# Performance work log

Hardware: AMD Instinct MI355X
Metric: run time of the kernel (lower is better)

Reference implementation:

```python
import jax, jax.numpy as jnp
import numpy as np


def setup_inputs() -> dict:
    key = jax.random.key(0)
    k1, k2 = jax.random.split(key)
    B, H, N, C = 8, 8, 2048, 64
    x = jax.random.normal(k1, (B, H, N, C), dtype=jnp.float32)
    # torch nn.Linear(dim, 3*dim) weight layout: [3C, C]
    W_qkv = jax.random.normal(k2, (3 * C, C), dtype=jnp.float32) * (C ** -0.5)
    return {"x": x, "W_qkv": W_qkv}


def reference(x, W_qkv):
    B, H, N, C = x.shape
    scale = C ** -0.5
    # fused qkv projection: x @ W^T, then split
    qkv = jnp.einsum('bhnc,dc->bhnd', x, W_qkv)  # [B,H,N,3C]
    q, k, v = jnp.split(qkv, 3, axis=-1)
    # full N x N score matrix (matches the naive original)
    attn = jnp.einsum('bhnc,bhmc->bhnm', q, k) * scale
    attn = jax.nn.softmax(attn, axis=-1)
    out = jnp.einsum('bhnm,bhmc->bhnc', attn, v)  # [B,H,N,C]
    # head-mixing shuffle: reshape(B,H,N,H,C//H).transpose(1,3).reshape(B,H,N,C)
    out = out.reshape(B, H, N, H, C // H)
    out = out.transpose(0, 3, 2, 1, 4)
    return out.reshape(B, H, N, C)
```

## Files before the change

### kernel.cpp

```cpp
#include <hip/hip_runtime.h>
#include <math.h>

#define BH    64
#define NSEQ  2048
#define CDIM  64
#define WSTR  72

typedef unsigned short ushort_t;
typedef __attribute__((ext_vector_type(8))) short short8;
typedef __attribute__((ext_vector_type(4))) float float4v;

__device__ __forceinline__ ushort_t f32_to_bf16_rne(float x) {
  unsigned int u = __float_as_uint(x);
  u += 0x7fffu + ((u >> 16) & 1u);
  return (ushort_t)(u >> 16);
}

__device__ __forceinline__ unsigned int cvtpk(float a, float b) {
  unsigned int r;
  asm("v_cvt_pk_bf16_f32 %0, %1, %2" : "=v"(r) : "v"(a), "v"(b));
  return r;
}

__device__ __forceinline__ void glds16(const ushort_t* g, ushort_t* l) {
  __builtin_amdgcn_global_load_lds(
      (const __attribute__((address_space(1))) void*)g,
      (__attribute__((address_space(3))) void*)l, 16, 0, 0);
}

__global__ __launch_bounds__(256) void qkv_proj_mfma(
    const float* __restrict__ x, const float* __restrict__ w,
    ushort_t* __restrict__ q, ushort_t* __restrict__ k,
    ushort_t* __restrict__ vt) {
  __shared__ ushort_t Wb[192 * WSTR];
  ushort_t* Sg = Wb;
  const int t = threadIdx.x;
  const int lane = t & 63, wv = t >> 6;
  const int quad = lane >> 4, l16 = lane & 15;
  const long rowbase = (long)blockIdx.x * 128;
  const int head  = (int)(rowbase >> 11);
  const int nbase = (int)(rowbase & 2047);

  for (int u = t; u < 1536; u += 256) {
    const int d = u >> 3, o8 = (u & 7) * 8;
    const float sc = (d < 64) ? 0.1803368801111244f : 1.0f;
    const float4 f0 = *reinterpret_cast<const float4*>(w + d * 64 + o8);
    const float4 f1 = *reinterpret_cast<const float4*>(w + d * 64 + o8 + 4);
    ushort_t tmp[8] __attribute__((aligned(16)));
    tmp[0] = f32_to_bf16_rne(f0.x * sc); tmp[1] = f32_to_bf16_rne(f0.y * sc);
    tmp[2] = f32_to_bf16_rne(f0.z * sc); tmp[3] = f32_to_bf16_rne(f0.w * sc);
    tmp[4] = f32_to_bf16_rne(f1.x * sc); tmp[5] = f32_to_bf16_rne(f1.y * sc);
    tmp[6] = f32_to_bf16_rne(f1.z * sc); tmp[7] = f32_to_bf16_rne(f1.w * sc);
    *reinterpret_cast<uint4*>(&Wb[d * WSTR + o8]) = *reinterpret_cast<const uint4*>(tmp);
  }
  __syncthreads();

  short8 xf[2][2];
#pragma unroll
  for (int tm = 0; tm < 2; ++tm)
#pragma unroll
    for (int kb = 0; kb < 2; ++kb) {
      const float* xp = x + (rowbase + wv * 32 + tm * 16 + l16) * 64 + kb * 32 + quad * 8;
      const float4 f0 = *reinterpret_cast<const float4*>(xp);
      const float4 f1 = *reinterpret_cast<const float4*>(xp + 4);
      ushort_t tmp[8] __attribute__((aligned(16)));
      tmp[0] = f32_to_bf16_rne(f0.x); tmp[1] = f32_to_bf16_rne(f0.y);
      tmp[2] = f32_to_bf16_rne(f0.z); tmp[3] = f32_to_bf16_rne(f0.w);
      tmp[4] = f32_to_bf16_rne(f1.x); tmp[5] = f32_to_bf16_rne(f1.y);
      tmp[6] = f32_to_bf16_rne(f1.z); tmp[7] = f32_to_bf16_rne(f1.w);
      xf[tm][kb] = *reinterpret_cast<const short8*>(tmp);
    }

  float4v aqk[8][2];
  float4v av[2][4];
#pragma unroll
  for (int nt = 0; nt < 8; ++nt)
#pragma unroll
    for (int tm = 0; tm < 2; ++tm)
#pragma unroll
      for (int r = 0; r < 4; ++r) aqk[nt][tm][r] = 0.f;
#pragma unroll
  for (int tm = 0; tm < 2; ++tm)
#pragma unroll
    for (int nt = 0; nt < 4; ++nt)
#pragma unroll
      for (int r = 0; r < 4; ++r) av[tm][nt][r] = 0.f;

#pragma unroll
  for (int kb = 0; kb < 2; ++kb) {
#pragma unroll
    for (int nt = 0; nt < 8; ++nt) {
      const short8 wf = *reinterpret_cast<const short8*>(
          &Wb[(nt * 16 + l16) * WSTR + kb * 32 + quad * 8]);
      aqk[nt][0] = __builtin_amdgcn_mfma_f32_16x16x32_bf16(wf, xf[0][kb], aqk[nt][0], 0, 0, 0);
      aqk[nt][1] = __builtin_amdgcn_mfma_f32_16x16x32_bf16(wf, xf[1][kb], aqk[nt][1], 0, 0, 0);
    }
#pragma unroll
    for (int nt = 0; nt < 4; ++nt) {
      const short8 wfv = *reinterpret_cast<const short8*>(
          &Wb[((128 + nt * 16) + l16) * WSTR + kb * 32 + quad * 8]);
      av[0][nt] = __builtin_amdgcn_mfma_f32_16x16x32_bf16(xf[0][kb], wfv, av[0][nt], 0, 0, 0);
      av[1][nt] = __builtin_amdgcn_mfma_f32_16x16x32_bf16(xf[1][kb], wfv, av[1][nt], 0, 0, 0);
    }
  }

  __syncthreads();

#pragma unroll
  for (int tm = 0; tm < 2; ++tm) {
    const int row = wv * 32 + tm * 16 + l16;
#pragma unroll
    for (int nt = 0; nt < 4; ++nt) {
      const int dchunk = nt * 2 + (quad >> 1);
      uint2 pk;
      pk.x = cvtpk(aqk[nt][tm][0], aqk[nt][tm][1]);
      pk.y = cvtpk(aqk[nt][tm][2], aqk[nt][tm][3]);
      *reinterpret_cast<uint2*>(
          &Sg[row * 64 + ((dchunk ^ (row & 7)) * 8) + (quad & 1) * 4]) = pk;
    }
  }
  __syncthreads();
#pragma unroll
  for (int i = 0; i < 4; ++i) {
    const int g = i * 256 + t;
    const int row = g >> 3, ch = g & 7;
    const uint4 v = *reinterpret_cast<const uint4*>(
        &Sg[row * 64 + ((ch ^ (row & 7)) * 8)]);
    *reinterpret_cast<uint4*>(q + (rowbase + row) * 64 + ch * 8) = v;
  }
  __syncthreads();

#pragma unroll
  for (int tm = 0; tm < 2; ++tm) {
    const int row = wv * 32 + tm * 16 + l16;
#pragma unroll
    for (int nt = 4; nt < 8; ++nt) {
      const int dchunk = (nt - 4) * 2 + (quad >> 1);
      uint2 pk;
      pk.x = cvtpk(aqk[nt][tm][0], aqk[nt][tm][1]);
      pk.y = cvtpk(aqk[nt][tm][2], aqk[nt][tm][3]);
      *reinterpret_cast<uint2*>(
          &Sg[row * 64 + ((dchunk ^ (row & 7)) * 8) + (quad & 1) * 4]) = pk;
    }
  }
  __syncthreads();
#pragma unroll
  for (int i = 0; i < 4; ++i) {
    const int g = i * 256 + t;
    const int row = g >> 3, ch = g & 7;
    const uint4 v = *reinterpret_cast<const uint4*>(
        &Sg[row * 64 + ((ch ^ (row & 7)) * 8)]);
    *reinterpret_cast<uint4*>(k + (rowbase + row) * 64 + ch * 8) = v;
  }
  __syncthreads();

#pragma unroll
  for (int tm = 0; tm < 2; ++tm)
#pragma unroll
    for (int nt = 0; nt < 4; ++nt) {
      const int c = nt * 16 + l16;
      const int nchunk = wv * 4 + tm * 2 + (quad >> 1);
      uint2 pk;
      pk.x = cvtpk(av[tm][nt][0], av[tm][nt][1]);
      pk.y = cvtpk(av[tm][nt][2], av[tm][nt][3]);
      *reinterpret_cast<uint2*>(
          &Sg[c * 128 + ((nchunk ^ (c & 15)) * 8) + (quad & 1) * 4]) = pk;
    }
  __syncthreads();
#pragma unroll
  for (int i = 0; i < 4; ++i) {
    const int g = i * 256 + t;
    const int c = g >> 4, ch = g & 15;
    const uint4 v = *reinterpret_cast<const uint4*>(
        &Sg[c * 128 + ((ch ^ (c & 15)) * 8)]);
    *reinterpret_cast<uint4*>(vt + (long)head * (64 * 2048) + (long)c * 2048 +
                              nbase + ch * 8) = v;
  }
}

__global__ __launch_bounds__(512, 4) void flash_attn_mfma(
    const ushort_t* __restrict__ q, const ushort_t* __restrict__ k,
    const ushort_t* __restrict__ vt, float* __restrict__ out) {
  __shared__ ushort_t Ks2[2][32 * 64];
  __shared__ ushort_t Vs2[2][64 * 32];
  __shared__ ushort_t Ps[256 * 32];
  const int t = threadIdx.x;
  const int lane = t & 63, w = t >> 6;
  const int quad = lane >> 4, l16 = lane & 15;
  const int id = blockIdx.x;
  const int qt = id >> 6;
  const int bh = ((id & 7) << 3) | ((id >> 3) & 7);
  const long hoff = (long)bh * NSEQ * CDIM;
  const ushort_t* qp  = q  + hoff + (long)qt * 256 * CDIM;
  const ushort_t* kp  = k  + hoff;
  const ushort_t* vtp = vt + hoff;

  short8 qf[2][2];
#pragma unroll
  for (int tm = 0; tm < 2; ++tm)
#pragma unroll
    for (int kb = 0; kb < 2; ++kb)
      qf[tm][kb] = *reinterpret_cast<const short8*>(
          qp + (w * 32 + tm * 16 + l16) * 64 + kb * 32 + quad * 8);

  float4v O[4][2];
  float rs[2];
  rs[0] = 0.f; rs[1] = 0.f;
#pragma unroll
  for (int ct = 0; ct < 4; ++ct)
#pragma unroll
    for (int tm = 0; tm < 2; ++tm)
#pragma unroll
      for (int r = 0; r < 4; ++r) O[ct][tm][r] = 0.f;

  const int ws = w & 3;
  const bool isK = (w < 4);
  const int krow = ws * 8 + (lane >> 3);
  const int kchk = (lane & 7) ^ (lane >> 3);
  const int kdst = ws * 8 * 64;
  const int vrow = ws * 16 + (lane >> 2);
  const int vchk = (lane & 3) ^ ((lane >> 3) & 3);
  const int vdst = ws * 16 * 32;
  const int pswz = (l16 >> 1) & 3;

  if (isK) glds16(kp + (long)krow * 64 + kchk * 8, &Ks2[0][kdst]);
  else     glds16(vtp + (long)vrow * 2048 + vchk * 8, &Vs2[0][vdst]);

  for (int tile = 0; tile < NSEQ / 32; ++tile) {
    const int cur = tile & 1;
    __syncthreads();
    if (tile < NSEQ / 32 - 1) {
      const long nxt = tile + 1;
      if (isK) glds16(kp + (nxt * 32 + krow) * 64 + kchk * 8, &Ks2[1 - cur][kdst]);
      else     glds16(vtp + (long)vrow * 2048 + nxt * 32 + vchk * 8, &Vs2[1 - cur][vdst]);
    }

    float4v s[2][2];
#pragma unroll
    for (int nt = 0; nt < 2; ++nt)
#pragma unroll
      for (int tm = 0; tm < 2; ++tm)
#pragma unroll
        for (int r = 0; r < 4; ++r) s[nt][tm][r] = 0.f;

#pragma unroll
    for (int kb = 0; kb < 2; ++kb) {
      short8 kf[2];
#pragma unroll
      for (int nt = 0; nt < 2; ++nt)
        kf[nt] = *reinterpret_cast<const short8*>(
            &Ks2[cur][(nt * 16 + l16) * 64 + (((kb * 4 + quad) ^ (l16 & 7)) * 8)]);
#pragma unroll
      for (int nt = 0; nt < 2; ++nt)
#pragma unroll
        for (int tm = 0; tm < 2; ++tm)
          s[nt][tm] = __builtin_amdgcn_mfma_f32_16x16x32_bf16(
              kf[nt], qf[tm][kb], s[nt][tm], 0, 0, 0);
    }

#pragma unroll
    for (int tm = 0; tm < 2; ++tm)
#pragma unroll
      for (int nt = 0; nt < 2; ++nt) {
        const float p0 = __builtin_amdgcn_exp2f(s[nt][tm][0]);
        const float p1 = __builtin_amdgcn_exp2f(s[nt][tm][1]);
        const float p2 = __builtin_amdgcn_exp2f(s[nt][tm][2]);
        const float p3 = __builtin_amdgcn_exp2f(s[nt][tm][3]);
        rs[tm] += (p0 + p1) + (p2 + p3);
        uint2 pk;
        pk.x = cvtpk(p0, p1);
        pk.y = cvtpk(p2, p3);
        *reinterpret_cast<uint2*>(
            &Ps[(w * 32 + tm * 16 + l16) * 32 +
                (((nt * 2 + (quad >> 1)) ^ pswz) * 8) + (quad & 1) * 4]) = pk;
      }

    {
      short8 pf[2], vf[4];
#pragma unroll
      for (int tm = 0; tm < 2; ++tm)
        pf[tm] = *reinterpret_cast<const short8*>(
            &Ps[(w * 32 + tm * 16 + l16) * 32 + ((quad ^ pswz) * 8)]);
#pragma unroll
      for (int ct = 0; ct < 4; ++ct)
        vf[ct] = *reinterpret_cast<const short8*>(
            &Vs2[cur][(ct * 16 + l16) * 32 + ((quad ^ pswz) * 8)]);
#pragma unroll
      for (int ct = 0; ct < 4; ++ct)
#pragma unroll
        for (int tm = 0; tm < 2; ++tm)
          O[ct][tm] = __builtin_amdgcn_mfma_f32_16x16x32_bf16(
              vf[ct], pf[tm], O[ct][tm], 0, 0, 0);
    }
  }

  const int bi = bh >> 3, h = bh & 7;
  float inv[2];
#pragma unroll
  for (int tm = 0; tm < 2; ++tm) {
    float l = rs[tm];
    l += __shfl_xor(l, 16, 64);
    l += __shfl_xor(l, 32, 64);
    inv[tm] = 1.f / l;
  }
#pragma unroll
  for (int ct = 0; ct < 4; ++ct)
#pragma unroll
    for (int tm = 0; tm < 2; ++tm) {
      const int n = qt * 256 + w * 32 + tm * 16 + l16;
      const int h2 = ct * 2 + (quad >> 1);
      const int c2b = (quad & 1) * 4;
      float4 v4;
      v4.x = O[ct][tm][0] * inv[tm]; v4.y = O[ct][tm][1] * inv[tm];
      v4.z = O[ct][tm][2] * inv[tm]; v4.w = O[ct][tm][3] * inv[tm];
      *reinterpret_cast<float4*>(
          &out[(((long)(bi * 8 + h2)) * NSEQ + n) * 64 + h * 8 + c2b]) = v4;
    }
}

extern "C" void kernel_launch(void* const* d_in, const int* in_sizes, int n_in,
                              void* d_out, int out_size, void* d_ws, size_t ws_size,
                              hipStream_t stream) {
  (void)in_sizes; (void)n_in; (void)out_size; (void)ws_size;
  const float* x = (const float*)d_in[0];
  const float* w = (const float*)d_in[1];
  float* out = (float*)d_out;

  ushort_t* qws  = (ushort_t*)d_ws;
  ushort_t* kws  = qws + (size_t)BH * NSEQ * CDIM;
  ushort_t* vtws = kws + (size_t)BH * NSEQ * CDIM;

  qkv_proj_mfma<<<(BH * NSEQ) / 128, 256, 0, stream>>>(x, w, qws, kws, vtws);
  flash_attn_mfma<<<512, 512, 0, stream>>>(qws, kws, vtws, out);
}
```

Baseline: 164.5 us.

## Precompute swizzled bf16 weight image once and async-load it; raise MFMA priority

Adds a tiny one-block kernel that converts, scales and XOR-swizzles W_qkv into a bf16 image once, stored in the tail of the output buffer, which the flash kernel later overwrites. Each of the 1024 projection blocks then copies that image straight into LDS with global_load_lds, overlapped with the x conversion, instead of converting fp32 weights per block. It also wraps the MFMA groups in the attention loop with s_setprio to favour matrix issue. The cost is an extra kernel launch and reliance on output-buffer scratch being overwritten later.

Result: no change. 166.1 us (+1.0%).

```diff
diff --git a/kernel.cpp b/kernel.cpp
--- a/kernel.cpp
+++ b/kernel.cpp
@@ -4,7 +4,6 @@
 #define BH    64
 #define NSEQ  2048
 #define CDIM  64
-#define WSTR  72
 
 typedef unsigned short ushort_t;
 typedef __attribute__((ext_vector_type(8))) short short8;
@@ -28,11 +27,30 @@
       (__attribute__((address_space(3))) void*)l, 16, 0, 0);
 }
 
+__global__ __launch_bounds__(256) void w_prep(
+    const float* __restrict__ w, ushort_t* __restrict__ wimg) {
+  const int t = threadIdx.x;
+#pragma unroll
+  for (int i = 0; i < 6; ++i) {
+    const int idx = i * 256 + t;
+    const int d = idx >> 3, ch = idx & 7;
+    const float sc = (d < 64) ? 0.1803368801111244f : 1.0f;
+    const float4 f0 = *reinterpret_cast<const float4*>(w + d * 64 + ch * 8);
+    const float4 f1 = *reinterpret_cast<const float4*>(w + d * 64 + ch * 8 + 4);
+    uint4 pk4;
+    pk4.x = cvtpk(f0.x * sc, f0.y * sc);
+    pk4.y = cvtpk(f0.z * sc, f0.w * sc);
+    pk4.z = cvtpk(f1.x * sc, f1.y * sc);
+    pk4.w = cvtpk(f1.z * sc, f1.w * sc);
+    *reinterpret_cast<uint4*>(wimg + d * 64 + ((ch ^ (d & 7)) * 8)) = pk4;
+  }
+}
+
 __global__ __launch_bounds__(256) void qkv_proj_mfma(
-    const float* __restrict__ x, const float* __restrict__ w,
+    const float* __restrict__ x, const ushort_t* __restrict__ wimg,
     ushort_t* __restrict__ q, ushort_t* __restrict__ k,
     ushort_t* __restrict__ vt) {
-  __shared__ ushort_t Wb[192 * WSTR];
+  __shared__ ushort_t Wb[192 * 64];
   ushort_t* Sg = Wb;
   const int t = threadIdx.x;
   const int lane = t & 63, wv = t >> 6;
@@ -41,19 +59,9 @@
   const int head  = (int)(rowbase >> 11);
   const int nbase = (int)(rowbase & 2047);
 
-  for (int u = t; u < 1536; u += 256) {
-    const int d = u >> 3, o8 = (u & 7) * 8;
-    const float sc = (d < 64) ? 0.1803368801111244f : 1.0f;
-    const float4 f0 = *reinterpret_cast<const float4*>(w + d * 64 + o8);
-    const float4 f1 = *reinterpret_cast<const float4*>(w + d * 64 + o8 + 4);
-    ushort_t tmp[8] __attribute__((aligned(16)));
-    tmp[0] = f32_to_bf16_rne(f0.x * sc); tmp[1] = f32_to_bf16_rne(f0.y * sc);
-    tmp[2] = f32_to_bf16_rne(f0.z * sc); tmp[3] = f32_to_bf16_rne(f0.w * sc);
-    tmp[4] = f32_to_bf16_rne(f1.x * sc); tmp[5] = f32_to_bf16_rne(f1.y * sc);
-    tmp[6] = f32_to_bf16_rne(f1.z * sc); tmp[7] = f32_to_bf16_rne(f1.w * sc);
-    *reinterpret_cast<uint4*>(&Wb[d * WSTR + o8]) = *reinterpret_cast<const uint4*>(tmp);
-  }
-  __syncthreads();
+#pragma unroll
+  for (int i = 0; i < 6; ++i)
+    glds16(wimg + (size_t)(i * 256 + t) * 8, &Wb[(i * 256 + wv * 64) * 8]);
 
   short8 xf[2][2];
 #pragma unroll
@@ -70,6 +78,7 @@
       tmp[6] = f32_to_bf16_rne(f1.z); tmp[7] = f32_to_bf16_rne(f1.w);
       xf[tm][kb] = *reinterpret_cast<const short8*>(tmp);
     }
+  __syncthreads();
 
   float4v aqk[8][2];
   float4v av[2][4];
@@ -90,15 +99,17 @@
   for (int kb = 0; kb < 2; ++kb) {
 #pragma unroll
     for (int nt = 0; nt < 8; ++nt) {
+      const int r = nt * 16 + l16;
       const short8 wf = *reinterpret_cast<const short8*>(
-          &Wb[(nt * 16 + l16) * WSTR + kb * 32 + quad * 8]);
+          &Wb[r * 64 + (((kb * 4 + quad) ^ (r & 7)) * 8)]);
       aqk[nt][0] = __builtin_amdgcn_mfma_f32_16x16x32_bf16(wf, xf[0][kb], aqk[nt][0], 0, 0, 0);
       aqk[nt][1] = __builtin_amdgcn_mfma_f32_16x16x32_bf16(wf, xf[1][kb], aqk[nt][1], 0, 0, 0);
     }
 #pragma unroll
     for (int nt = 0; nt < 4; ++nt) {
+      const int r = 128 + nt * 16 + l16;
       const short8 wfv = *reinterpret_cast<const short8*>(
-          &Wb[((128 + nt * 16) + l16) * WSTR + kb * 32 + quad * 8]);
+          &Wb[r * 64 + (((kb * 4 + quad) ^ (r & 7)) * 8)]);
       av[0][nt] = __builtin_amdgcn_mfma_f32_16x16x32_bf16(xf[0][kb], wfv, av[0][nt], 0, 0, 0);
       av[1][nt] = __builtin_amdgcn_mfma_f32_16x16x32_bf16(xf[1][kb], wfv, av[1][nt], 0, 0, 0);
     }
@@ -250,12 +261,14 @@
       for (int nt = 0; nt < 2; ++nt)
         kf[nt] = *reinterpret_cast<const short8*>(
             &Ks2[cur][(nt * 16 + l16) * 64 + (((kb * 4 + quad) ^ (l16 & 7)) * 8)]);
+      __builtin_amdgcn_s_setprio(1);
 #pragma unroll
       for (int nt = 0; nt < 2; ++nt)
 #pragma unroll
         for (int tm = 0; tm < 2; ++tm)
           s[nt][tm] = __builtin_amdgcn_mfma_f32_16x16x32_bf16(
               kf[nt], qf[tm][kb], s[nt][tm], 0, 0, 0);
+      __builtin_amdgcn_s_setprio(0);
     }
 
 #pragma unroll
@@ -285,12 +298,14 @@
       for (int ct = 0; ct < 4; ++ct)
         vf[ct] = *reinterpret_cast<const short8*>(
             &Vs2[cur][(ct * 16 + l16) * 32 + ((quad ^ pswz) * 8)]);
+      __builtin_amdgcn_s_setprio(1);
 #pragma unroll
       for (int ct = 0; ct < 4; ++ct)
 #pragma unroll
         for (int tm = 0; tm < 2; ++tm)
           O[ct][tm] = __builtin_amdgcn_mfma_f32_16x16x32_bf16(
               vf[ct], pf[tm], O[ct][tm], 0, 0, 0);
+      __builtin_amdgcn_s_setprio(0);
     }
   }
 
@@ -330,6 +345,9 @@
   ushort_t* kws  = qws + (size_t)BH * NSEQ * CDIM;
   ushort_t* vtws = kws + (size_t)BH * NSEQ * CDIM;
 
-  qkv_proj_mfma<<<(BH * NSEQ) / 128, 256, 0, stream>>>(x, w, qws, kws, vtws);
+  ushort_t* wimg = (ushort_t*)(out + (size_t)8 * 8 * 2048 * 64 - 6144);
+
+  w_prep<<<1, 256, 0, stream>>>(w, wimg);
+  qkv_proj_mfma<<<(BH * NSEQ) / 128, 256, 0, stream>>>(x, wimg, qws, kws, vtws);
   flash_attn_mfma<<<512, 512, 0, stream>>>(qws, kws, vtws, out);
 }
```

## Process two row tiles per QKV projection block with prefetched x loads

Applied to the files above, without the earlier changes.

Each QKV projection block now handles 256 rows as two 128-row tiles, so the bf16 conversion of W into shared memory is paid half as often. The next tile's x values are loaded into registers before the current tile's output stores, overlapping global load latency with the shuffle and write-back. A separate Sg staging buffer replaces the aliasing of Wb. In exchange the kernel uses more shared memory and registers, and the grid has half as many blocks. The projection is a small share of total time next to the attention kernel.

Result: slower. 169.1 us (+2.9%).

```diff
diff --git a/kernel.cpp b/kernel.cpp
--- a/kernel.cpp
+++ b/kernel.cpp
@@ -33,13 +33,11 @@
     ushort_t* __restrict__ q, ushort_t* __restrict__ k,
     ushort_t* __restrict__ vt) {
   __shared__ ushort_t Wb[192 * WSTR];
-  ushort_t* Sg = Wb;
+  __shared__ ushort_t Sg[128 * 64];
   const int t = threadIdx.x;
   const int lane = t & 63, wv = t >> 6;
   const int quad = lane >> 4, l16 = lane & 15;
-  const long rowbase = (long)blockIdx.x * 128;
-  const int head  = (int)(rowbase >> 11);
-  const int nbase = (int)(rowbase & 2047);
+  const long rb0 = (long)blockIdx.x * 256;
 
   for (int u = t; u < 1536; u += 256) {
     const int d = u >> 3, o8 = (u & 7) * 8;
@@ -53,14 +51,13 @@
     tmp[6] = f32_to_bf16_rne(f1.z * sc); tmp[7] = f32_to_bf16_rne(f1.w * sc);
     *reinterpret_cast<uint4*>(&Wb[d * WSTR + o8]) = *reinterpret_cast<const uint4*>(tmp);
   }
-  __syncthreads();
 
   short8 xf[2][2];
 #pragma unroll
   for (int tm = 0; tm < 2; ++tm)
 #pragma unroll
     for (int kb = 0; kb < 2; ++kb) {
-      const float* xp = x + (rowbase + wv * 32 + tm * 16 + l16) * 64 + kb * 32 + quad * 8;
+      const float* xp = x + (rb0 + wv * 32 + tm * 16 + l16) * 64 + kb * 32 + quad * 8;
       const float4 f0 = *reinterpret_cast<const float4*>(xp);
       const float4 f1 = *reinterpret_cast<const float4*>(xp + 4);
       ushort_t tmp[8] __attribute__((aligned(16)));
@@ -70,111 +67,147 @@
       tmp[6] = f32_to_bf16_rne(f1.z); tmp[7] = f32_to_bf16_rne(f1.w);
       xf[tm][kb] = *reinterpret_cast<const short8*>(tmp);
     }
-
-  float4v aqk[8][2];
-  float4v av[2][4];
-#pragma unroll
-  for (int nt = 0; nt < 8; ++nt)
+  __syncthreads();
+
+#pragma unroll
+  for (int tile = 0; tile < 2; ++tile) {
+    const long rowbase = rb0 + (long)tile * 128;
+    const int head  = (int)(rowbase >> 11);
+    const int nbase = (int)(rowbase & 2047);
+
+    float4v aqk[8][2];
+    float4v av[2][4];
+#pragma unroll
+    for (int nt = 0; nt < 8; ++nt)
+#pragma unroll
+      for (int tm = 0; tm < 2; ++tm)
+#pragma unroll
+        for (int r = 0; r < 4; ++r) aqk[nt][tm][r] = 0.f;
 #pragma unroll
     for (int tm = 0; tm < 2; ++tm)
 #pragma unroll
-      for (int r = 0; r < 4; ++r) aqk[nt][tm][r] = 0.f;
-#pragma unroll
-  for (int tm = 0; tm < 2; ++tm)
-#pragma unroll
-    for (int nt = 0; nt < 4; ++nt)
-#pragma unroll
-      for (int r = 0; r < 4; ++r) av[tm][nt][r] = 0.f;
-
-#pragma unroll
-  for (int kb = 0; kb < 2; ++kb) {
-#pragma unroll
-    for (int nt = 0; nt < 8; ++nt) {
-      const short8 wf = *reinterpret_cast<const short8*>(
-          &Wb[(nt * 16 + l16) * WSTR + kb * 32 + quad * 8]);
-      aqk[nt][0] = __builtin_amdgcn_mfma_f32_16x16x32_bf16(wf, xf[0][kb], aqk[nt][0], 0, 0, 0);
-      aqk[nt][1] = __builtin_amdgcn_mfma_f32_16x16x32_bf16(wf, xf[1][kb], aqk[nt][1], 0, 0, 0);
-    }
-#pragma unroll
-    for (int nt = 0; nt < 4; ++nt) {
-      const short8 wfv = *reinterpret_cast<const short8*>(
-          &Wb[((128 + nt * 16) + l16) * WSTR + kb * 32 + quad * 8]);
-      av[0][nt] = __builtin_amdgcn_mfma_f32_16x16x32_bf16(xf[0][kb], wfv, av[0][nt], 0, 0, 0);
-      av[1][nt] = __builtin_amdgcn_mfma_f32_16x16x32_bf16(xf[1][kb], wfv, av[1][nt], 0, 0, 0);
-    }
-  }
-
-  __syncthreads();
-
-#pragma unroll
-  for (int tm = 0; tm < 2; ++tm) {
-    const int row = wv * 32 + tm * 16 + l16;
-#pragma unroll
-    for (int nt = 0; nt < 4; ++nt) {
-      const int dchunk = nt * 2 + (quad >> 1);
-      uint2 pk;
-      pk.x = cvtpk(aqk[nt][tm][0], aqk[nt][tm][1]);
-      pk.y = cvtpk(aqk[nt][tm][2], aqk[nt][tm][3]);
-      *reinterpret_cast<uint2*>(
-          &Sg[row * 64 + ((dchunk ^ (row & 7)) * 8) + (quad & 1) * 4]) = pk;
-    }
-  }
-  __syncthreads();
-#pragma unroll
-  for (int i = 0; i < 4; ++i) {
-    const int g = i * 256 + t;
-    const int row = g >> 3, ch = g & 7;
-    const uint4 v = *reinterpret_cast<const uint4*>(
-        &Sg[row * 64 + ((ch ^ (row & 7)) * 8)]);
-    *reinterpret_cast<uint4*>(q + (rowbase + row) * 64 + ch * 8) = v;
-  }
-  __syncthreads();
-
-#pragma unroll
-  for (int tm = 0; tm < 2; ++tm) {
-    const int row = wv * 32 + tm * 16 + l16;
-#pragma unroll
-    for (int nt = 4; nt < 8; ++nt) {
-      const int dchunk = (nt - 4) * 2 + (quad >> 1);
-      uint2 pk;
-      pk.x = cvtpk(aqk[nt][tm][0], aqk[nt][tm][1]);
-      pk.y = cvtpk(aqk[nt][tm][2], aqk[nt][tm][3]);
-      *reinterpret_cast<uint2*>(
-          &Sg[row * 64 + ((dchunk ^ (row & 7)) * 8) + (quad & 1) * 4]) = pk;
-    }
-  }
-  __syncthreads();
-#pragma unroll
-  for (int i = 0; i < 4; ++i) {
-    const int g = i * 256 + t;
-    const int row = g >> 3, ch = g & 7;
-    const uint4 v = *reinterpret_cast<const uint4*>(
-        &Sg[row * 64 + ((ch ^ (row & 7)) * 8)]);
-    *reinterpret_cast<uint4*>(k + (rowbase + row) * 64 + ch * 8) = v;
-  }
-  __syncthreads();
-
-#pragma unroll
-  for (int tm = 0; tm < 2; ++tm)
-#pragma unroll
-    for (int nt = 0; nt < 4; ++nt) {
-      const int c = nt * 16 + l16;
-      const int nchunk = wv * 4 + tm * 2 + (quad >> 1);
-      uint2 pk;
-      pk.x = cvtpk(av[tm][nt][0], av[tm][nt][1]);
-      pk.y = cvtpk(av[tm][nt][2], av[tm][nt][3]);
-      *reinterpret_cast<uint2*>(
-          &Sg[c * 128 + ((nchunk ^ (c & 15)) * 8) + (quad & 1) * 4]) = pk;
-    }
-  __syncthreads();
-#pragma unroll
-  for (int i = 0; i < 4; ++i) {
-    const int g = i * 256 + t;
-    const int c = g >> 4, ch = g & 15;
-    const uint4 v = *reinterpret_cast<const uint4*>(
-        &Sg[c * 128 + ((ch ^ (c & 15)) * 8)]);
-    *reinterpret_cast<uint4*>(vt + (long)head * (64 * 2048) + (long)c * 2048 +
-                              nbase + ch * 8) = v;
+      for (int nt = 0; nt < 4; ++nt)
+#pragma unroll
+        for (int r = 0; r < 4; ++r) av[tm][nt][r] = 0.f;
+
+#pragma unroll
+    for (int kb = 0; kb < 2; ++kb) {
+#pragma unroll
+      for (int nt = 0; nt < 8; ++nt) {
+        const short8 wf = *reinterpret_cast<const short8*>(
+            &Wb[(nt * 16 + l16) * WSTR + kb * 32 + quad * 8]);
+        aqk[nt][0] = __builtin_amdgcn_mfma_f32_16x16x32_bf16(wf, xf[0][kb], aqk[nt][0], 0, 0, 0);
+        aqk[nt][1] = __builtin_amdgcn_mfma_f32_16x16x32_bf16(wf, xf[1][kb], aqk[nt][1], 0, 0, 0);
+      }
+#pragma unroll
+      for (int nt = 0; nt < 4; ++nt) {
+        const short8 wfv = *reinterpret_cast<const short8*>(
+            &Wb[((128 + nt * 16) + l16) * WSTR + kb * 32 + quad * 8]);
+        av[0][nt] = __builtin_amdgcn_mfma_f32_16x16x32_bf16(xf[0][kb], wfv, av[0][nt], 0, 0, 0);
+        av[1][nt] = __builtin_amdgcn_mfma_f32_16x16x32_bf16(xf[1][kb], wfv, av[1][nt], 0, 0, 0);
+      }
+    }
+
+    float4 nx[8];
+    if (tile == 0) {
+#pragma unroll
+      for (int tm = 0; tm < 2; ++tm)
+#pragma unroll
+        for (int kb = 0; kb < 2; ++kb) {
+          const float* xp = x + (rb0 + 128 + wv * 32 + tm * 16 + l16) * 64 + kb * 32 + quad * 8;
+          nx[(tm * 2 + kb) * 2]     = *reinterpret_cast<const float4*>(xp);
+          nx[(tm * 2 + kb) * 2 + 1] = *reinterpret_cast<const float4*>(xp + 4);
+        }
+    }
+
+    __syncthreads();
+
+#pragma unroll
+    for (int tm = 0; tm < 2; ++tm) {
+      const int row = wv * 32 + tm * 16 + l16;
+#pragma unroll
+      for (int nt = 0; nt < 4; ++nt) {
+        const int dchunk = nt * 2 + (quad >> 1);
+        uint2 pk;
+        pk.x = cvtpk(aqk[nt][tm][0], aqk[nt][tm][1]);
+        pk.y = cvtpk(aqk[nt][tm][2], aqk[nt][tm][3]);
+        *reinterpret_cast<uint2*>(
+            &Sg[row * 64 + ((dchunk ^ (row & 7)) * 8) + (quad & 1) * 4]) = pk;
+      }
+    }
+    __syncthreads();
+#pragma unroll
+    for (int i = 0; i < 4; ++i) {
+      const int g = i * 256 + t;
+      const int row = g >> 3, ch = g & 7;
+      const uint4 v = *reinterpret_cast<const uint4*>(
+          &Sg[row * 64 + ((ch ^ (row & 7)) * 8)]);
+      *reinterpret_cast<uint4*>(q + (rowbase + row) * 64 + ch * 8) = v;
+    }
+    __syncthreads();
+
+#pragma unroll
+    for (int tm = 0; tm < 2; ++tm) {
+      const int row = wv * 32 + tm * 16 + l16;
+#pragma unroll
+      for (int nt = 4; nt < 8; ++nt) {
+        const int dchunk = (nt - 4) * 2 + (quad >> 1);
+        uint2 pk;
+        pk.x = cvtpk(aqk[nt][tm][0], aqk[nt][tm][1]);
+        pk.y = cvtpk(aqk[nt][tm][2], aqk[nt][tm][3]);
+        *reinterpret_cast<uint2*>(
+            &Sg[row * 64 + ((dchunk ^ (row & 7)) * 8) + (quad & 1) * 4]) = pk;
+      }
+    }
+    __syncthreads();
+#pragma unroll
+    for (int i = 0; i < 4; ++i) {
+      const int g = i * 256 + t;
+      const int row = g >> 3, ch = g & 7;
+      const uint4 v = *reinterpret_cast<const uint4*>(
+          &Sg[row * 64 + ((ch ^ (row & 7)) * 8)]);
+      *reinterpret_cast<uint4*>(k + (rowbase + row) * 64 + ch * 8) = v;
+    }
+    __syncthreads();
+
+#pragma unroll
+    for (int tm = 0; tm < 2; ++tm)
+#pragma unroll
+      for (int nt = 0; nt < 4; ++nt) {
+        const int c = nt * 16 + l16;
+        const int nchunk = wv * 4 + tm * 2 + (quad >> 1);
+        uint2 pk;
+        pk.x = cvtpk(av[tm][nt][0], av[tm][nt][1]);
+        pk.y = cvtpk(av[tm][nt][2], av[tm][nt][3]);
+        *reinterpret_cast<uint2*>(
+            &Sg[c * 128 + ((nchunk ^ (c & 15)) * 8) + (quad & 1) * 4]) = pk;
+      }
+    __syncthreads();
+#pragma unroll
+    for (int i = 0; i < 4; ++i) {
+      const int g = i * 256 + t;
+      const int c = g >> 4, ch = g & 15;
+      const uint4 v = *reinterpret_cast<const uint4*>(
+          &Sg[c * 128 + ((ch ^ (c & 15)) * 8)]);
+      *reinterpret_cast<uint4*>(vt + (long)head * (64 * 2048) + (long)c * 2048 +
+                                nbase + ch * 8) = v;
+    }
+
+    if (tile == 0) {
+#pragma unroll
+      for (int tm = 0; tm < 2; ++tm)
+#pragma unroll
+        for (int kb = 0; kb < 2; ++kb) {
+          const float4 f0 = nx[(tm * 2 + kb) * 2];
+          const float4 f1 = nx[(tm * 2 + kb) * 2 + 1];
+          ushort_t tmp[8] __attribute__((aligned(16)));
+          tmp[0] = f32_to_bf16_rne(f0.x); tmp[1] = f32_to_bf16_rne(f0.y);
+          tmp[2] = f32_to_bf16_rne(f0.z); tmp[3] = f32_to_bf16_rne(f0.w);
+          tmp[4] = f32_to_bf16_rne(f1.x); tmp[5] = f32_to_bf16_rne(f1.y);
+          tmp[6] = f32_to_bf16_rne(f1.z); tmp[7] = f32_to_bf16_rne(f1.w);
+          xf[tm][kb] = *reinterpret_cast<const short8*>(tmp);
+        }
+    }
   }
 }
 
@@ -330,6 +363,6 @@
   ushort_t* kws  = qws + (size_t)BH * NSEQ * CDIM;
   ushort_t* vtws = kws + (size_t)BH * NSEQ * CDIM;
 
-  qkv_proj_mfma<<<(BH * NSEQ) / 128, 256, 0, stream>>>(x, w, qws, kws, vtws);
+  qkv_proj_mfma<<<(BH * NSEQ) / 256, 256, 0, stream>>>(x, w, qws, kws, vtws);
   flash_attn_mfma<<<512, 512, 0, stream>>>(qws, kws, vtws, out);
 }
```
